# Optimization experiments

Measured on AMD Instinct MI355X. Metric: run time of the kernel, lower is better.

Reference implementation:

```python
import jax, jax.numpy as jnp
import numpy as np

B, S, H = 2, 512, 1024
D = 24            # hdim_proj_dim
MLP_H = 96        # hdim_mlp_hidden
VAL_IN = 2 * H    # concat_only
OUT_HID = 2 * max(128, H // 2)  # 1024


def setup_inputs() -> dict:
    key = jax.random.key(0)
    ks = jax.random.split(key, 12)
    sc = 0.02
    return {
        "H_j": jax.random.normal(ks[0], (B, S, H), jnp.float32),
        "H_i": jax.random.normal(ks[1], (B, S, H), jnp.float32),
        "attn_mask": jnp.ones((B, S), jnp.float32),
        "p_j": jax.random.normal(ks[2], (H, D), jnp.float32) * sc,
        "p_i": jax.random.normal(ks[3], (H, D), jnp.float32) * sc,
        "W1": jax.random.normal(ks[4], (4 * D, MLP_H), jnp.float32) * sc,
        "b1": jnp.zeros((MLP_H,), jnp.float32),
        "W2": jax.random.normal(ks[5], (MLP_H, 1), jnp.float32) * sc,
        "b2": jnp.zeros((1,), jnp.float32),
        "Wv1": jax.random.normal(ks[6], (VAL_IN, OUT_HID), jnp.float32) * sc,
        "bv1": jnp.zeros((OUT_HID,), jnp.float32),
        "Wv2": jax.random.normal(ks[7], (OUT_HID, H), jnp.float32) * sc,
        "bv2": jnp.zeros((H,), jnp.float32),
        "alpha": jnp.asarray(0.05, jnp.float32),
    }


def reference(H_j, H_i, attn_mask, p_j, p_i, W1, b1, W2, b2, Wv1, bv1, Wv2, bv2, alpha):
    # Low-dim projections: [B,S,D]
    Zj = jnp.einsum('bsh,hd->bsd', H_j, p_j)
    Zi = jnp.einsum('bsh,hd->bsd', H_i, p_i)
    # 4-term pairwise features: [B,S,S,4D]
    Zj_b = jnp.broadcast_to(Zj[:, :, None, :], (B, S, S, D))
    Zi_b = jnp.broadcast_to(Zi[:, None, :, :], (B, S, S, D))
    pair = jnp.concatenate([Zj_b, Zi_b, Zj_b * Zi_b, jnp.abs(Zj_b - Zi_b)], axis=-1)
    # Pair-score MLP -> logits [B,S,S]
    h = jax.nn.relu(jnp.einsum('bjif,fm->bjim', pair, W1) + b1)
    logits = (jnp.einsum('bjim,mo->bjio', h, W2) + b2)[..., 0]
    # additive key-side mask (same as torch _expand_mask_last)
    logits = logits + (1.0 - attn_mask)[:, None, :] * jnp.finfo(logits.dtype).min
    # token_temp == 1.0 -> no scaling
    probs = jax.nn.softmax(logits, axis=-1)  # over keys i
    ctx = jnp.einsum('bji,bih->bjh', probs, H_i)  # [B,S,H]
    # Value fusion MLP (concat_only), dropout is identity in eval
    msg_in = jnp.concatenate([ctx, H_j], axis=-1)  # [B,S,2H]
    msg = jax.nn.relu(jnp.einsum('bsf,fo->bso', msg_in, Wv1) + bv1)
    msg = jnp.einsum('bso,oh->bsh', msg, Wv2) + bv2
    return alpha * msg
```

## Files before the change

### kernel.cpp

```cpp
#include <hip/hip_runtime.h>
#include <math.h>

#define B_    2
#define S_    512
#define HDIM  1024
#define D_    24
#define M_    96
#define ROWS  (B_*S_)

typedef _Float16 half8 __attribute__((ext_vector_type(8)));
typedef float    f32x4 __attribute__((ext_vector_type(4)));
typedef unsigned short ushort8 __attribute__((ext_vector_type(8)));

__device__ __forceinline__ void transpose_tile64_cache(
    const float* __restrict__ in, _Float16* __restrict__ out,
    int R, int C, int xt, int yt, int t) {
  int R0 = yt * 64, C0 = xt * 64;
  int c = t >> 2, rq = (t & 3) * 16;
  _Float16 o[16];
  const float* src = in + (size_t)(R0 + rq) * C + C0 + c;
#pragma unroll
  for (int e = 0; e < 16; ++e) o[e] = (_Float16)src[(size_t)e * C];
  _Float16* dst = out + (size_t)(C0 + c) * R + R0 + rq;
  *(ushort8*)dst = *(ushort8*)o;
  *(ushort8*)(dst + 8) = *(ushort8*)&o[8];
}

__global__ __launch_bounds__(256) void prep_kernel(
    const float* __restrict__ Hi, const float* __restrict__ pj,
    const float* __restrict__ pi, const float* __restrict__ W1,
    const float* __restrict__ Wv1, const float* __restrict__ Wv2,
    _Float16* __restrict__ HiT, _Float16* __restrict__ Wv1T,
    _Float16* __restrict__ Wv2T, _Float16* __restrict__ Wimg,
    _Float16* __restrict__ PjT, _Float16* __restrict__ PiT) {
  const int bid = blockIdx.x;
  const int t = threadIdx.x;

  if (bid < 4) {
    int c = bid * 256 + t;
    half8 v = {};
    if (c < 864) {
      int kc = c / 96, m = c - kc * 96;
#pragma unroll
      for (int e = 0; e < 8; ++e)
        v[e] = (_Float16)W1[(24 + kc * 8 + e) * M_ + m];
    }
    *(half8*)(Wimg + (size_t)c * 8) = v;
  } else if (bid < 12) {
    int id = bid - 4;
    const float* P = (id < 4) ? pj : pi;
    _Float16* PT = (id < 4) ? PjT : PiT;
    int k = (id & 3) * 256 + t;
#pragma unroll
    for (int d = 0; d < 32; ++d) {
      float v = (d < D_) ? P[(size_t)k * D_ + d] : 0.0f;
      PT[(size_t)d * 1024 + k] = (_Float16)v;
    }
  } else if (bid < 268) {
    int id = bid - 12;
    int z = id >> 7, rem = id & 127;
    transpose_tile64_cache(Hi + (size_t)z * S_ * HDIM,
                           HiT + (size_t)z * HDIM * S_,
                           S_, HDIM, rem & 15, rem >> 4, t);
  } else if (bid < 780) {
    int id = bid - 268;
    transpose_tile64_cache(Wv1, Wv1T, 2 * HDIM, HDIM, id & 15, id >> 4, t);
  } else {
    int id = bid - 780;
    transpose_tile64_cache(Wv2, Wv2T, HDIM, HDIM, id & 15, id >> 4, t);
  }
}

__global__ __launch_bounds__(64) void proj_kernel(
    const float* __restrict__ Hj, const float* __restrict__ Hi,
    const _Float16* __restrict__ PjT, const _Float16* __restrict__ PiT,
    _Float16* __restrict__ HjH, float* __restrict__ Zj,
    float* __restrict__ Zi) {
  const int bid = blockIdx.x;
  const int l = threadIdx.x;
  const int lo = l & 15, hi = l >> 4;
  const bool isj = bid < 64;
  const int r0 = (bid & 63) * 16;
  const float* H = isj ? Hj : Hi;
  const _Float16* PT = isj ? PjT : PiT;
  float* Z = isj ? Zj : Zi;
  const float* hrow = H + (size_t)(r0 + lo) * HDIM;

  f32x4 acc0 = {}, acc1 = {};
  for (int step = 0; step < 32; ++step) {
    const float* src = hrow + step * 32 + hi * 8;
    float4 v0 = *(const float4*)src;
    float4 v1 = *(const float4*)(src + 4);
    half8 a8;
    a8[0] = (_Float16)v0.x; a8[1] = (_Float16)v0.y;
    a8[2] = (_Float16)v0.z; a8[3] = (_Float16)v0.w;
    a8[4] = (_Float16)v1.x; a8[5] = (_Float16)v1.y;
    a8[6] = (_Float16)v1.z; a8[7] = (_Float16)v1.w;
    if (isj)
      *(half8*)(HjH + (size_t)(r0 + lo) * HDIM + step * 32 + hi * 8) = a8;
    half8 b0 = *(const half8*)(PT + (size_t)lo * 1024 + step * 32 + hi * 8);
    half8 b1 = *(const half8*)(PT + (size_t)(16 + lo) * 1024 + step * 32 + hi * 8);
    acc0 = __builtin_amdgcn_mfma_f32_16x16x32_f16(a8, b0, acc0, 0, 0, 0);
    acc1 = __builtin_amdgcn_mfma_f32_16x16x32_f16(a8, b1, acc1, 0, 0, 0);
  }
#pragma unroll
  for (int rg = 0; rg < 4; ++rg) {
    int row = r0 + hi * 4 + rg;
    Z[(size_t)row * D_ + lo] = acc0[rg];
    if (lo < 8) Z[(size_t)row * D_ + 16 + lo] = acc1[rg];
  }
}

#define FOFFB   0
#define WOFFB   40960
#define ZOFFB   (WOFFB + 960*16)
#define LOGOFFB (WOFFB + 16384)
#define ZJOFFB  (LOGOFFB + 2048)
#define W2OFFB  (ZJOFFB + 96)
#define REDOFFB (W2OFFB + 384)
#define LDSB    (REDOFFB + 32)

__global__ __launch_bounds__(256) void pair_fused_kernel(
    const float* __restrict__ Zj, const float* __restrict__ Zi,
    const float* __restrict__ W1, const float* __restrict__ b1,
    const float* __restrict__ W2, const _Float16* __restrict__ Wimg,
    const float* __restrict__ mask, _Float16* __restrict__ probs) {
  __shared__ __attribute__((aligned(16))) char smem[LDSB];
  const int t = threadIdx.x;
  const int w = t >> 6, l = t & 63;
  const int lo = l & 15, hi = l >> 4;
  const int rj = blockIdx.x;
  const int b = rj >> 9;

#pragma unroll
  for (int r = 0; r < 4; ++r) {
    const _Float16* src = Wimg + (size_t)(r * 256 + w * 64 + l) * 8;
    __builtin_amdgcn_global_load_lds(
        (const __attribute__((address_space(1))) void*)src,
        (__attribute__((address_space(3))) void*)(smem + WOFFB + (r * 256 + w * 64) * 16),
        16, 0, 0);
  }
  float* zjL    = (float*)(smem + ZJOFFB);
  float* W2s    = (float*)(smem + W2OFFB);
  float* logits = (float*)(smem + LOGOFFB);
  float* red    = (float*)(smem + REDOFFB);
  if (t < D_) zjL[t] = Zj[(size_t)rj * D_ + t];
  if (t < M_) W2s[t] = W2[t];
  float aj = 0.f;
  if (t < M_) {
    aj = b1[t];
#pragma unroll
    for (int d = 0; d < D_; ++d)
      aj = fmaf(Zj[(size_t)rj * D_ + d], W1[d * M_ + t], aj);
  }
  __syncthreads();
  if (t < M_) {
    half8 v = {};
    v[0] = (_Float16)aj;
    *(half8*)(smem + WOFFB + (864 + t) * 16) = v;
  }

  half8 wf[6][3];
  float w2r[6][4];

  for (int p = 0; p < 2; ++p) {
    {
      int i = p * 256 + t;
      const float* zi = Zi + (size_t)(b * S_ + i) * D_;
      float ziv[D_];
#pragma unroll
      for (int q = 0; q < 6; ++q) {
        float4 v = ((const float4*)zi)[q];
        ziv[q * 4 + 0] = v.x; ziv[q * 4 + 1] = v.y;
        ziv[q * 4 + 2] = v.z; ziv[q * 4 + 3] = v.w;
      }
#pragma unroll
      for (int kc = 0; kc < 3; ++kc) {
        half8 v;
#pragma unroll
        for (int e = 0; e < 8; ++e) v[e] = (_Float16)ziv[kc * 8 + e];
        *(half8*)(smem + FOFFB + (kc * 256 + t) * 16) = v;
      }
#pragma unroll
      for (int kc = 0; kc < 3; ++kc) {
        half8 v;
#pragma unroll
        for (int e = 0; e < 8; ++e) {
          int d = kc * 8 + e;
          v[e] = (_Float16)(zjL[d] * ziv[d]);
        }
        *(half8*)(smem + FOFFB + ((kc + 3) * 256 + t) * 16) = v;
      }
#pragma unroll
      for (int kc = 0; kc < 3; ++kc) {
        half8 v;
#pragma unroll
        for (int e = 0; e < 8; ++e) {
          int d = kc * 8 + e;
          v[e] = (_Float16)fabsf(zjL[d] - ziv[d]);
        }
        *(half8*)(smem + FOFFB + ((kc + 6) * 256 + t) * 16) = v;
      }
      if (p == 0) {
        half8 v = {};
        v[0] = (_Float16)1.0f;
        *(half8*)(smem + FOFFB + (9 * 256 + t) * 16) = v;
      }
    }
    __syncthreads();

    if (p == 0) {
#pragma unroll
      for (int mh = 0; mh < 6; ++mh) {
#pragma unroll
        for (int ks = 0; ks < 3; ++ks) {
          int kc = ks * 4 + hi;
          int off = (kc < 10) ? (WOFFB + (kc * 96 + mh * 16 + lo) * 16) : ZOFFB;
          wf[mh][ks] = *(const half8*)(smem + off);
        }
#pragma unroll
        for (int r = 0; r < 4; ++r) w2r[mh][r] = W2s[mh * 16 + hi * 4 + r];
      }
    }

#pragma unroll
    for (int nt = 0; nt < 4; ++nt) {
      half8 ff[3];
#pragma unroll
      for (int ks = 0; ks < 3; ++ks) {
        int kc = ks * 4 + hi;
        int off = (kc < 10) ? (FOFFB + (kc * 256 + w * 64 + nt * 16 + lo) * 16) : ZOFFB;
        ff[ks] = *(const half8*)(smem + off);
      }
      f32x4 a6[6] = {};
      __builtin_amdgcn_s_setprio(1);
#pragma unroll
      for (int ks = 0; ks < 3; ++ks)
#pragma unroll
        for (int mh = 0; mh < 6; ++mh)
          a6[mh] = __builtin_amdgcn_mfma_f32_16x16x32_f16(wf[mh][ks], ff[ks], a6[mh], 0, 0, 0);
      __builtin_amdgcn_s_setprio(0);
      float part = 0.f;
#pragma unroll
      for (int mh = 0; mh < 6; ++mh)
#pragma unroll
        for (int r = 0; r < 4; ++r)
          part = fmaf(fmaxf(a6[mh][r], 0.f), w2r[mh][r], part);
      part += __shfl_xor(part, 16);
      part += __shfl_xor(part, 32);
      if (hi == 0) logits[p * 256 + w * 64 + nt * 16 + lo] = part;
    }
    __syncthreads();
  }

  float m1 = mask[b * S_ + t], m2 = mask[b * S_ + t + 256];
  float lg1 = logits[t]       + (1.0f - m1) * (-3.40282347e38f);
  float lg2 = logits[t + 256] + (1.0f - m2) * (-3.40282347e38f);
  float mx = fmaxf(lg1, lg2);
#pragma unroll
  for (int off = 32; off > 0; off >>= 1) mx = fmaxf(mx, __shfl_xor(mx, off));
  if (l == 0) red[w] = mx;
  __syncthreads();
  float rmax = fmaxf(fmaxf(red[0], red[1]), fmaxf(red[2], red[3]));
  float e1 = __expf(lg1 - rmax);
  float e2 = __expf(lg2 - rmax);
  float s = e1 + e2;
#pragma unroll
  for (int off = 32; off > 0; off >>= 1) s += __shfl_xor(s, off);
  if (l == 0) red[4 + w] = s;
  __syncthreads();
  float inv = 1.0f / (red[4] + red[5] + red[6] + red[7]);
  probs[(size_t)rj * S_ + t]       = (_Float16)(e1 * inv);
  probs[(size_t)rj * S_ + t + 256] = (_Float16)(e2 * inv);
}

template <bool HASA1, bool RELU, bool FINAL, bool OUTH>
__global__ __launch_bounds__(512) void mfma_gemm_kernel(
    const _Float16* __restrict__ A0, const _Float16* __restrict__ A1,
    const _Float16* __restrict__ Bt, const float* __restrict__ bias,
    const float* __restrict__ alpha_ptr, void* __restrict__ Cout,
    int M, int N, int K0, int K1,
    long aB0, long aB1, long bB, long cB) {
  __shared__ __attribute__((aligned(16))) char smem[65536];
  const int t = threadIdx.x;
  const int w = t >> 6, l = t & 63;
  const int g = w >> 2, wq = w & 3;
  const int K = K0 + K1;
  const int KH = K >> 1;
  const int NT = KH >> 5;
  const int n0 = blockIdx.x * 64, m0 = blockIdx.y * 64;
  const int zb = blockIdx.z;
  const _Float16* A0b = A0 + (size_t)zb * aB0;
  const _Float16* A1b = HASA1 ? (A1 + (size_t)zb * aB1) : nullptr;
  const _Float16* Btb = Bt + (size_t)zb * bB;
  char* gls = smem + (g << 15);

  const int sr = (wq << 4) + (l >> 2);
  const int sk = ((l & 3) ^ ((l >> 3) & 3)) << 3;

  const int mq = wq >> 1, nq = wq & 1;
  int offA[2], offB[2];
#pragma unroll
  for (int i = 0; i < 2; ++i) {
    int ra = mq * 32 + i * 16 + (l & 15);
    offA[i] = ra * 64 + (((l >> 4) ^ ((ra >> 1) & 3)) << 4);
    int rb = nq * 32 + i * 16 + (l & 15);
    offB[i] = 4096 + rb * 64 + (((l >> 4) ^ ((rb >> 1) & 3)) << 4);
  }

  f32x4 acc[2][2] = {};

  auto stage = [&](int tt) {
    char* buf = gls + (tt & 3) * 8192;
    int kg = g * KH + (tt << 5) + sk;
    const _Float16* ga;
    if (HASA1 && kg >= K0) ga = A1b + (size_t)(m0 + sr) * K1 + (kg - K0);
    else                   ga = A0b + (size_t)(m0 + sr) * K0 + kg;
    __builtin_amdgcn_global_load_lds(
        (const __attribute__((address_space(1))) void*)ga,
        (__attribute__((address_space(3))) void*)(buf + (wq << 10)), 16, 0, 0);
    const _Float16* gb = Btb + (size_t)(n0 + sr) * K + kg;
    __builtin_amdgcn_global_load_lds(
        (const __attribute__((address_space(1))) void*)gb,
        (__attribute__((address_space(3))) void*)(buf + 4096 + (wq << 10)), 16, 0, 0);
  };

  stage(0);
  stage(1);
  stage(2);

  for (int tt = 0; tt < NT; ++tt) {
    if (tt + 2 < NT)      asm volatile("s_waitcnt vmcnt(4)" ::: "memory");
    else if (tt + 1 < NT) asm volatile("s_waitcnt vmcnt(2)" ::: "memory");
    else                  asm volatile("s_waitcnt vmcnt(0)" ::: "memory");
    __builtin_amdgcn_s_barrier();
    __builtin_amdgcn_sched_barrier(0);
    const char* buf = gls + (tt & 3) * 8192;
    half8 a0 = *(const half8*)(buf + offA[0]);
    half8 a1 = *(const half8*)(buf + offA[1]);
    half8 b0 = *(const half8*)(buf + offB[0]);
    half8 b1v = *(const half8*)(buf + offB[1]);
    acc[0][0] = __builtin_amdgcn_mfma_f32_16x16x32_f16(a0, b0, acc[0][0], 0, 0, 0);
    acc[0][1] = __builtin_amdgcn_mfma_f32_16x16x32_f16(a0, b1v, acc[0][1], 0, 0, 0);
    acc[1][0] = __builtin_amdgcn_mfma_f32_16x16x32_f16(a1, b0, acc[1][0], 0, 0, 0);
    acc[1][1] = __builtin_amdgcn_mfma_f32_16x16x32_f16(a1, b1v, acc[1][1], 0, 0, 0);
    if (tt + 3 < NT) stage(tt + 3);
  }

  const int lr = l & 15, lq = l >> 4;
  float* redm = (float*)smem;
  __syncthreads();
  if (g == 1) {
#pragma unroll
    for (int mi = 0; mi < 2; ++mi)
#pragma unroll
      for (int ni = 0; ni < 2; ++ni)
#pragma unroll
        for (int rg = 0; rg < 4; ++rg)
          redm[(mq * 32 + mi * 16 + lq * 4 + rg) * 68 + nq * 32 + ni * 16 + lr] =
              acc[mi][ni][rg];
  }
  __syncthreads();
  if (g == 0) {
    const float alpha = FINAL ? *alpha_ptr : 1.0f;
    const size_t cbase = (size_t)zb * cB;
#pragma unroll
    for (int mi = 0; mi < 2; ++mi)
#pragma unroll
      for (int ni = 0; ni < 2; ++ni) {
        int col = n0 + nq * 32 + ni * 16 + lr;
        float bv = bias ? bias[col] : 0.0f;
#pragma unroll
        for (int rg = 0; rg < 4; ++rg) {
          int row = m0 + mq * 32 + mi * 16 + lq * 4 + rg;
          float x = acc[mi][ni][rg] +
                    redm[(mq * 32 + mi * 16 + lq * 4 + rg) * 68 + nq * 32 + ni * 16 + lr] +
                    bv;
          if (RELU) x = fmaxf(x, 0.f);
          if (FINAL) x *= alpha;
          if (OUTH)
            ((_Float16*)Cout)[cbase + (size_t)row * N + col] = (_Float16)x;
          else
            ((float*)Cout)[cbase + (size_t)row * N + col] = x;
        }
      }
  }
}

extern "C" void kernel_launch(void* const* d_in, const int* in_sizes, int n_in,
                              void* d_out, int out_size, void* d_ws, size_t ws_size,
                              hipStream_t stream) {
  const float* Hj   = (const float*)d_in[0];
  const float* Hi   = (const float*)d_in[1];
  const float* mask = (const float*)d_in[2];
  const float* pj   = (const float*)d_in[3];
  const float* pi   = (const float*)d_in[4];
  const float* W1   = (const float*)d_in[5];
  const float* b1   = (const float*)d_in[6];
  const float* W2   = (const float*)d_in[7];
  const float* Wv1  = (const float*)d_in[9];
  const float* bv1  = (const float*)d_in[10];
  const float* Wv2  = (const float*)d_in[11];
  const float* bv2  = (const float*)d_in[12];
  const float* alpha = (const float*)d_in[13];

  char* w = (char*)d_ws;
  float* Zj  = (float*)w;            w += (size_t)ROWS * D_ * 4;
  float* Zi  = (float*)w;            w += (size_t)ROWS * D_ * 4;
  _Float16* Wimg   = (_Float16*)w;   w += (size_t)1024 * 16;
  _Float16* PjT    = (_Float16*)w;   w += (size_t)32 * 1024 * 2;
  _Float16* PiT    = (_Float16*)w;   w += (size_t)32 * 1024 * 2;
  _Float16* probsH = (_Float16*)w;   w += (size_t)B_ * S_ * S_ * 2;
  _Float16* HjH    = (_Float16*)w;   w += (size_t)ROWS * HDIM * 2;
  _Float16* HiT    = (_Float16*)w;   w += (size_t)B_ * HDIM * S_ * 2;
  _Float16* Wv1T   = (_Float16*)w;   w += (size_t)HDIM * 2 * HDIM * 2;
  _Float16* Wv2T   = (_Float16*)w;   w += (size_t)HDIM * HDIM * 2;
  _Float16* ctxH   = (_Float16*)w;   w += (size_t)ROWS * HDIM * 2;
  _Float16* hidH   = (_Float16*)w;   w += (size_t)ROWS * HDIM * 2;
  float* out = (float*)d_out;

  prep_kernel<<<1036, 256, 0, stream>>>(Hi, pj, pi, W1, Wv1, Wv2,
                                        HiT, Wv1T, Wv2T, Wimg, PjT, PiT);
  proj_kernel<<<128, 64, 0, stream>>>(Hj, Hi, PjT, PiT, HjH, Zj, Zi);

  pair_fused_kernel<<<ROWS, 256, 0, stream>>>(Zj, Zi, W1, b1, W2, Wimg,
                                              mask, probsH);

  mfma_gemm_kernel<false, false, false, true><<<dim3(16, 8, 2), 512, 0, stream>>>(
      probsH, nullptr, HiT, nullptr, nullptr, ctxH,
      S_, HDIM, S_, 0, (long)S_ * S_, 0, (long)HDIM * S_, (long)S_ * HDIM);
  mfma_gemm_kernel<true, true, false, true><<<dim3(16, 16, 1), 512, 0, stream>>>(
      ctxH, HjH, Wv1T, bv1, nullptr, hidH,
      ROWS, HDIM, HDIM, HDIM, 0, 0, 0, 0);
  mfma_gemm_kernel<false, false, true, false><<<dim3(16, 16, 1), 512, 0, stream>>>(
      hidH, nullptr, Wv2T, bv2, alpha, out,
      ROWS, HDIM, HDIM, 0, 0, 0, 0, 0);
}
```

Measured before the change: 76.07 us.

## Fold low-dim projection into prep kernel with LDS-staged projection weights

Removes the separate proj_kernel launch and the PjT/PiT global transposes. The Hj/Hi projections now run inside prep_kernel, with each block converting p_j/p_i straight into an LDS fragment layout and computing 64 rows across 4 waves. This saves one launch and one global round trip, at the cost of 32KB of static LDS on every prep block, which can lower occupancy for the transpose blocks. Each projection block also redundantly reconverts the full projection matrix from global memory.

New measurement: 68.52 us. -9.9%, faster.

```diff
diff --git a/kernel.cpp b/kernel.cpp
--- a/kernel.cpp
+++ b/kernel.cpp
@@ -26,18 +26,79 @@
   *(ushort8*)(dst + 8) = *(ushort8*)&o[8];
 }
 
+template <bool EMITH>
+__device__ __forceinline__ void proj_mfma64(
+    const float* __restrict__ H, const float* __restrict__ P,
+    float* __restrict__ Z, _Float16* __restrict__ Himg,
+    int r0, char* smem, int t) {
+  const int w = t >> 6, l = t & 63;
+  const int lo = l & 15, hi = l >> 4;
+  const int row = r0 + w * 16 + lo;
+  const float* hrow = H + (size_t)row * HDIM;
+  f32x4 acc0 = {}, acc1 = {};
+
+  for (int ph = 0; ph < 2; ++ph) {
+    if (ph) __syncthreads();
+    for (int q = 0; q < 8; ++q) {
+      int s = t + q * 256;
+      int slo = s & 15, shi = (s >> 4) & 3, snt = (s >> 6) & 1, sst = s >> 7;
+      int d = snt * 16 + slo;
+      half8 v = {};
+      if (d < D_) {
+        int k = (ph * 16 + sst) * 32 + shi * 8;
+#pragma unroll
+        for (int e = 0; e < 8; ++e)
+          v[e] = (_Float16)P[(size_t)(k + e) * D_ + d];
+      }
+      *(half8*)(smem + s * 16) = v;
+    }
+    __syncthreads();
+
+    for (int st = 0; st < 16; ++st) {
+      int step = ph * 16 + st;
+      const float* src = hrow + step * 32 + hi * 8;
+      float4 v0 = *(const float4*)src;
+      float4 v1 = *(const float4*)(src + 4);
+      half8 a8;
+      a8[0] = (_Float16)v0.x; a8[1] = (_Float16)v0.y;
+      a8[2] = (_Float16)v0.z; a8[3] = (_Float16)v0.w;
+      a8[4] = (_Float16)v1.x; a8[5] = (_Float16)v1.y;
+      a8[6] = (_Float16)v1.z; a8[7] = (_Float16)v1.w;
+      if (EMITH)
+        *(half8*)(Himg + (size_t)row * HDIM + step * 32 + hi * 8) = a8;
+      half8 b0 = *(const half8*)(smem + ((st * 2 + 0) * 64 + l) * 16);
+      half8 b1 = *(const half8*)(smem + ((st * 2 + 1) * 64 + l) * 16);
+      acc0 = __builtin_amdgcn_mfma_f32_16x16x32_f16(a8, b0, acc0, 0, 0, 0);
+      acc1 = __builtin_amdgcn_mfma_f32_16x16x32_f16(a8, b1, acc1, 0, 0, 0);
+    }
+  }
+#pragma unroll
+  for (int rg = 0; rg < 4; ++rg) {
+    int zr = r0 + w * 16 + hi * 4 + rg;
+    Z[(size_t)zr * D_ + lo] = acc0[rg];
+    if (lo < 8) Z[(size_t)zr * D_ + 16 + lo] = acc1[rg];
+  }
+}
+
 __global__ __launch_bounds__(256) void prep_kernel(
-    const float* __restrict__ Hi, const float* __restrict__ pj,
-    const float* __restrict__ pi, const float* __restrict__ W1,
-    const float* __restrict__ Wv1, const float* __restrict__ Wv2,
-    _Float16* __restrict__ HiT, _Float16* __restrict__ Wv1T,
-    _Float16* __restrict__ Wv2T, _Float16* __restrict__ Wimg,
-    _Float16* __restrict__ PjT, _Float16* __restrict__ PiT) {
+    const float* __restrict__ Hj, const float* __restrict__ Hi,
+    const float* __restrict__ pj, const float* __restrict__ pi,
+    const float* __restrict__ W1, const float* __restrict__ Wv1,
+    const float* __restrict__ Wv2,
+    _Float16* __restrict__ HjH, _Float16* __restrict__ HiT,
+    _Float16* __restrict__ Wv1T, _Float16* __restrict__ Wv2T,
+    _Float16* __restrict__ Wimg, float* __restrict__ Zj,
+    float* __restrict__ Zi) {
+  __shared__ __attribute__((aligned(16))) char smem[32768];
   const int bid = blockIdx.x;
   const int t = threadIdx.x;
 
-  if (bid < 4) {
-    int c = bid * 256 + t;
+  if (bid < 16) {
+    proj_mfma64<true>(Hj, pj, Zj, HjH, bid * 64, smem, t);
+  } else if (bid < 32) {
+    proj_mfma64<false>(Hi, pi, Zi, nullptr, (bid - 16) * 64, smem, t);
+  } else if (bid < 36) {
+    int c = (bid - 32) * 256 + t;
     half8 v = {};
     if (c < 864) {
       int kc = c / 96, m = c - kc * 96;
@@ -46,68 +107,18 @@
         v[e] = (_Float16)W1[(24 + kc * 8 + e) * M_ + m];
     }
     *(half8*)(Wimg + (size_t)c * 8) = v;
-  } else if (bid < 12) {
-    int id = bid - 4;
-    const float* P = (id < 4) ? pj : pi;
-    _Float16* PT = (id < 4) ? PjT : PiT;
-    int k = (id & 3) * 256 + t;
-#pragma unroll
-    for (int d = 0; d < 32; ++d) {
-      float v = (d < D_) ? P[(size_t)k * D_ + d] : 0.0f;
-      PT[(size_t)d * 1024 + k] = (_Float16)v;
-    }
-  } else if (bid < 268) {
-    int id = bid - 12;
+  } else if (bid < 292) {
+    int id = bid - 36;
     int z = id >> 7, rem = id & 127;
     transpose_tile64_cache(Hi + (size_t)z * S_ * HDIM,
                            HiT + (size_t)z * HDIM * S_,
                            S_, HDIM, rem & 15, rem >> 4, t);
-  } else if (bid < 780) {
-    int id = bid - 268;
+  } else if (bid < 804) {
+    int id = bid - 292;
     transpose_tile64_cache(Wv1, Wv1T, 2 * HDIM, HDIM, id & 15, id >> 4, t);
   } else {
-    int id = bid - 780;
+    int id = bid - 804;
     transpose_tile64_cache(Wv2, Wv2T, HDIM, HDIM, id & 15, id >> 4, t);
-  }
-}
-
-__global__ __launch_bounds__(64) void proj_kernel(
-    const float* __restrict__ Hj, const float* __restrict__ Hi,
-    const _Float16* __restrict__ PjT, const _Float16* __restrict__ PiT,
-    _Float16* __restrict__ HjH, float* __restrict__ Zj,
-    float* __restrict__ Zi) {
-  const int bid = blockIdx.x;
-  const int l = threadIdx.x;
-  const int lo = l & 15, hi = l >> 4;
-  const bool isj = bid < 64;
-  const int r0 = (bid & 63) * 16;
-  const float* H = isj ? Hj : Hi;
-  const _Float16* PT = isj ? PjT : PiT;
-  float* Z = isj ? Zj : Zi;
-  const float* hrow = H + (size_t)(r0 + lo) * HDIM;
-
-  f32x4 acc0 = {}, acc1 = {};
-  for (int step = 0; step < 32; ++step) {
-    const float* src = hrow + step * 32 + hi * 8;
-    float4 v0 = *(const float4*)src;
-    float4 v1 = *(const float4*)(src + 4);
-    half8 a8;
-    a8[0] = (_Float16)v0.x; a8[1] = (_Float16)v0.y;
-    a8[2] = (_Float16)v0.z; a8[3] = (_Float16)v0.w;
-    a8[4] = (_Float16)v1.x; a8[5] = (_Float16)v1.y;
-    a8[6] = (_Float16)v1.z; a8[7] = (_Float16)v1.w;
-    if (isj)
-      *(half8*)(HjH + (size_t)(r0 + lo) * HDIM + step * 32 + hi * 8) = a8;
-    half8 b0 = *(const half8*)(PT + (size_t)lo * 1024 + step * 32 + hi * 8);
-    half8 b1 = *(const half8*)(PT + (size_t)(16 + lo) * 1024 + step * 32 + hi * 8);
-    acc0 = __builtin_amdgcn_mfma_f32_16x16x32_f16(a8, b0, acc0, 0, 0, 0);
-    acc1 = __builtin_amdgcn_mfma_f32_16x16x32_f16(a8, b1, acc1, 0, 0, 0);
-  }
-#pragma unroll
-  for (int rg = 0; rg < 4; ++rg) {
-    int row = r0 + hi * 4 + rg;
-    Z[(size_t)row * D_ + lo] = acc0[rg];
-    if (lo < 8) Z[(size_t)row * D_ + 16 + lo] = acc1[rg];
   }
 }
 
@@ -408,8 +419,6 @@
   float* Zj  = (float*)w;            w += (size_t)ROWS * D_ * 4;
   float* Zi  = (float*)w;            w += (size_t)ROWS * D_ * 4;
   _Float16* Wimg   = (_Float16*)w;   w += (size_t)1024 * 16;
-  _Float16* PjT    = (_Float16*)w;   w += (size_t)32 * 1024 * 2;
-  _Float16* PiT    = (_Float16*)w;   w += (size_t)32 * 1024 * 2;
   _Float16* probsH = (_Float16*)w;   w += (size_t)B_ * S_ * S_ * 2;
   _Float16* HjH    = (_Float16*)w;   w += (size_t)ROWS * HDIM * 2;
   _Float16* HiT    = (_Float16*)w;   w += (size_t)B_ * HDIM * S_ * 2;
@@ -419,9 +428,8 @@
   _Float16* hidH   = (_Float16*)w;   w += (size_t)ROWS * HDIM * 2;
   float* out = (float*)d_out;
 
-  prep_kernel<<<1036, 256, 0, stream>>>(Hi, pj, pi, W1, Wv1, Wv2,
-                                        HiT, Wv1T, Wv2T, Wimg, PjT, PiT);
-  proj_kernel<<<128, 64, 0, stream>>>(Hj, Hi, PjT, PiT, HjH, Zj, Zi);
+  prep_kernel<<<1060, 256, 0, stream>>>(Hj, Hi, pj, pi, W1, Wv1, Wv2,
+                                        HjH, HiT, Wv1T, Wv2T, Wimg, Zj, Zi);
 
   pair_fused_kernel<<<ROWS, 256, 0, stream>>>(Zj, Zi, W1, b1, W2, Wimg,
                                               mask, probsH);
```
